# Performance work log

Hardware: AMD Instinct MI355X
Metric: run time of the kernel (lower is better)

## Reference

```python
import jax, jax.numpy as jnp
import numpy as np

D = 128      # input_dim (= out_channels = edge_dim)
H = 2        # n_head
N_ENT = 100000
B = 64       # number of queries / batches
R = 500      # number of relations
E = 400000   # number of original edges
NEG = 0.2    # GATv2 leaky_relu negative slope


def setup_inputs() -> dict:
    key = jax.random.key(0)
    ks = jax.random.split(key, 10)
    s = 1.0 / np.sqrt(D)
    queries = jax.random.normal(ks[0], (B, D), jnp.float32)
    entities = jax.random.normal(ks[1], (N_ENT, D), jnp.float32)
    edge_index = jax.random.randint(ks[2], (2, E), 0, N_ENT)
    relations = jax.random.normal(ks[3], (R, D), jnp.float32)
    relation_index = jax.random.randint(ks[4], (E,), 0, R)
    # guarantees batch.max()+1 == queries.shape[0] (module assert)
    batch = jnp.arange(N_ENT, dtype=jnp.int32) % B
    # GATv2Conv params: lin_l / lin_r (bias=True), lin_edge (bias=False), att, bias
    W_l = jax.random.normal(ks[5], (H * D, D), jnp.float32) * s
    b_l = jnp.zeros((H * D,), jnp.float32)
    W_r = jax.random.normal(ks[6], (H * D, D), jnp.float32) * s
    b_r = jnp.zeros((H * D,), jnp.float32)
    W_ea = jax.random.normal(ks[7], (H * D, D), jnp.float32) * s
    att = jax.random.normal(ks[8], (H, D), jnp.float32) * s
    bias = jnp.zeros((D,), jnp.float32)  # concat=False -> size out_channels
    # outer Injector.lin_edge: Linear(H*D, D, bias=True)
    W_le = jax.random.normal(ks[9], (D, H * D), jnp.float32) / np.sqrt(H * D)
    b_le = jnp.zeros((D,), jnp.float32)
    return dict(queries=queries, entities=entities, edge_index=edge_index,
                relations=relations, relation_index=relation_index, batch=batch,
                W_l=W_l, b_l=b_l, W_r=W_r, b_r=b_r, W_ea=W_ea, att=att,
                bias=bias, W_le=W_le, b_le=b_le)


def reference(queries, entities, edge_index, relations, relation_index, batch,
              W_l, b_l, W_r, b_r, W_ea, att, bias, W_le, b_le):
    n_ent = entities.shape[0]
    node = jnp.vstack([entities, queries])                        # [N+B, D]
    rel_feat = jnp.vstack([relations,
                           jnp.ones((1, relations.shape[1]), relations.dtype)])
    # added edges: query -> its entities
    src = jnp.concatenate([edge_index[0], batch.astype(edge_index.dtype) + n_ent])
    tgt = jnp.concatenate([edge_index[1],
                           jnp.arange(n_ent, dtype=edge_index.dtype)])
    rel_idx = jnp.concatenate([relation_index,
                               jnp.full((n_ent,), rel_feat.shape[0] - 1,
                                        relation_index.dtype)])
    edge_attr = rel_feat[rel_idx]                                  # [Etot, D]

    n_tot = node.shape[0]
    x_l = (node @ W_l.T + b_l).reshape(n_tot, H, D)                # source proj
    x_r = (node @ W_r.T + b_r).reshape(n_tot, H, D)                # target proj
    e = (edge_attr @ W_ea.T).reshape(-1, H, D)                     # [Etot, H, D]

    xj = x_l[src]                                                  # gather per edge
    z = jax.nn.leaky_relu(xj + x_r[tgt] + e, NEG)                  # [Etot, H, D]
    alpha = jnp.einsum('ehd,hd->eh', z, att)                       # [Etot, H]
    # segment softmax over target nodes
    amax = jax.ops.segment_max(alpha, tgt, num_segments=n_tot)
    alpha = jnp.exp(alpha - amax[tgt])
    denom = jax.ops.segment_sum(alpha, tgt, num_segments=n_tot)
    alpha = alpha / (denom[tgt] + 1e-16)

    msg = xj * alpha[..., None]                                    # [Etot, H, D]
    agg = jax.ops.segment_sum(msg, tgt, num_segments=n_tot)        # [Ntot, H, D]
    out = agg.mean(axis=1) + bias                                  # concat=False
    out_node = out[:n_ent]

    out_edge = jax.nn.relu(relations @ W_ea.T)                     # [R, H*D]
    out_edge = out_edge @ W_le.T + b_le                            # [R, D]
    return (out_node, out_edge)
```

## Files before the change

### kernel.cpp

```cpp
#include <hip/hip_runtime.h>
#include <math.h>

#define D 128
#define HD 256
#define N_ENT 100000
#define NBATCH 64
#define NTOT (N_ENT + NBATCH)
#define RCOUNT 500
#define E_BASE 400000
#define ETOT (E_BASE + N_ENT)
#define NEG 0.2f
#define SCAN_NB 391

typedef __attribute__((ext_vector_type(8))) short bf16x8;
typedef __attribute__((ext_vector_type(8))) unsigned short u16x8;
typedef __attribute__((ext_vector_type(4))) float f32x4;

static __device__ __forceinline__ unsigned short f2bf(float f) {
  unsigned u = __builtin_bit_cast(unsigned, f);
  u += 0x7fffu + ((u >> 16) & 1u);
  return (unsigned short)(u >> 16);
}
static __device__ __forceinline__ float bf2f(unsigned short h) {
  return __builtin_bit_cast(float, (unsigned)h << 16);
}

__global__ __launch_bounds__(256) void k_wcast(
    const float* __restrict__ W_l, const float* __restrict__ W_r,
    unsigned short* __restrict__ Wbf) {
  int idx = blockIdx.x * 256 + threadIdx.x;
  int e4 = idx * 4;
  int v = e4 >> 7;
  int k = e4 & 127;
  const float* src = (v < HD) ? (W_l + (size_t)v * D + k) : (W_r + (size_t)(v - HD) * D + k);
  float4 a = *(const float4*)src;
  *(ushort4*)(Wbf + (size_t)v * D + k) = make_ushort4(f2bf(a.x), f2bf(a.y), f2bf(a.z), f2bf(a.w));
}

__global__ __launch_bounds__(256) void k_rel(
    const float* __restrict__ relations, const float* __restrict__ W_ea,
    const float* __restrict__ W_le, const float* __restrict__ b_le,
    unsigned short* __restrict__ e_rel, float* __restrict__ out_edge) {
  __shared__ float relu_p[HD];
  int r = blockIdx.x;
  int j = threadIdx.x;
  const float* w = W_ea + (size_t)j * D;
  float acc = 0.f;
  if (r < RCOUNT) {
    const float* rel = relations + (size_t)r * D;
    for (int k = 0; k < D; k += 4) {
      float4 a = *(const float4*)(rel + k);
      float4 b = *(const float4*)(w + k);
      acc += a.x * b.x + a.y * b.y + a.z * b.z + a.w * b.w;
    }
  } else {
    for (int k = 0; k < D; k += 4) {
      float4 b = *(const float4*)(w + k);
      acc += b.x + b.y + b.z + b.w;
    }
  }
  e_rel[(size_t)r * HD + j] = f2bf(acc);
  if (r < RCOUNT) {
    relu_p[j] = acc > 0.f ? acc : 0.f;
    __syncthreads();
    if (j < D) {
      const float* wl = W_le + (size_t)j * HD;
      float o = b_le[j];
      for (int k = 0; k < HD; k += 4) {
        float4 p4 = *(const float4*)(relu_p + k);
        float4 w4 = *(const float4*)(wl + k);
        o += p4.x * w4.x + p4.y * w4.y + p4.z * w4.z + p4.w * w4.w;
      }
      out_edge[(size_t)r * D + j] = o;
    }
  }
}

#define LDA 136

__global__ __launch_bounds__(256) void k_gemm_mfma(
    const float* __restrict__ entities, const float* __restrict__ queries,
    const unsigned short* __restrict__ Wbf,
    const float* __restrict__ b_l, const float* __restrict__ b_r,
    unsigned short* __restrict__ x_l, unsigned short* __restrict__ x_r) {
  __shared__ unsigned short As[64 * LDA];
  __shared__ unsigned short Cs[64 * LDA];
  int rb = blockIdx.x;
  int gy = blockIdx.y;
  int tid = threadIdx.x;

  {
    int rr = tid >> 2;
    int part = (tid & 3) * 32;
    int row = rb * 64 + rr;
    const float* sp;
    if (row < N_ENT) sp = entities + (size_t)row * D;
    else if (row < NTOT) sp = queries + (size_t)(row - N_ENT) * D;
    else sp = entities;
#pragma unroll
    for (int k = 0; k < 32; k += 8) {
      float4 a0 = *(const float4*)(sp + part + k);
      float4 a1 = *(const float4*)(sp + part + k + 4);
      u16x8 p;
      p[0] = f2bf(a0.x); p[1] = f2bf(a0.y); p[2] = f2bf(a0.z); p[3] = f2bf(a0.w);
      p[4] = f2bf(a1.x); p[5] = f2bf(a1.y); p[6] = f2bf(a1.z); p[7] = f2bf(a1.w);
      *(u16x8*)(&As[rr * LDA + part + k]) = p;
    }
  }
  __syncthreads();

  int w = tid >> 6, lane = tid & 63;
  int wr = w >> 1, wc = w & 1;
  int m = lane & 15, q8 = (lane >> 4) * 8;
  const float* bv = gy ? b_r : b_l;
  unsigned short* xdst = gy ? x_r : x_l;

  for (int cc = 0; cc < 2; cc++) {
    f32x4 acc[2][4];
#pragma unroll
    for (int i = 0; i < 2; i++)
#pragma unroll
      for (int j = 0; j < 4; j++) acc[i][j] = (f32x4){0.f, 0.f, 0.f, 0.f};

    const unsigned short* wbase = Wbf + (size_t)(gy * 256 + cc * 128 + wc * 64 + m) * D;
#pragma unroll
    for (int ks = 0; ks < 128; ks += 32) {
      bf16x8 af[2], bfr[4];
#pragma unroll
      for (int i = 0; i < 2; i++)
        af[i] = *(const bf16x8*)(&As[(wr * 32 + i * 16 + m) * LDA + ks + q8]);
#pragma unroll
      for (int j = 0; j < 4; j++)
        bfr[j] = *(const bf16x8*)(wbase + (size_t)j * 16 * D + ks + q8);
#pragma unroll
      for (int i = 0; i < 2; i++)
#pragma unroll
        for (int j = 0; j < 4; j++)
          acc[i][j] = __builtin_amdgcn_mfma_f32_16x16x32_bf16(af[i], bfr[j], acc[i][j], 0, 0, 0);
    }

    __syncthreads();
#pragma unroll
    for (int j = 0; j < 4; j++) {
      int col = wc * 64 + j * 16 + m;
      float bb = bv[cc * 128 + col];
#pragma unroll
      for (int i = 0; i < 2; i++) {
        int row0 = wr * 32 + i * 16 + (lane >> 4) * 4;
#pragma unroll
        for (int r = 0; r < 4; r++)
          Cs[(row0 + r) * LDA + col] = f2bf(acc[i][j][r] + bb);
      }
    }
    __syncthreads();
#pragma unroll
    for (int it = 0; it < 4; it++) {
      int g = it * 256 + tid;
      int row = g >> 4, c8 = (g & 15) * 8;
      int grow = rb * 64 + row;
      if (grow < NTOT) {
        u16x8 v = *(const u16x8*)(&Cs[row * LDA + c8]);
        *(u16x8*)(xdst + (size_t)grow * HD + cc * 128 + c8) = v;
      }
    }
  }
}

__global__ void k_zero(int* __restrict__ counts) {
  int i = blockIdx.x * 256 + threadIdx.x;
  if (i < N_ENT) counts[i] = 0;
}

__global__ void k_hist(const int* __restrict__ edge_index, int* __restrict__ counts) {
  int e = blockIdx.x * 256 + threadIdx.x;
  if (e >= ETOT) return;
  int t = (e < E_BASE) ? edge_index[E_BASE + e] : (e - E_BASE);
  atomicAdd(counts + t, 1);
}

__global__ void k_scan1(const int* __restrict__ counts, int* __restrict__ bsum) {
  __shared__ int sdata[256];
  int i = blockIdx.x * 256 + threadIdx.x;
  sdata[threadIdx.x] = (i < N_ENT) ? counts[i] : 0;
  __syncthreads();
  for (int off = 128; off > 0; off >>= 1) {
    if (threadIdx.x < off) sdata[threadIdx.x] += sdata[threadIdx.x + off];
    __syncthreads();
  }
  if (threadIdx.x == 0) bsum[blockIdx.x] = sdata[0];
}

__global__ void k_scan2(const int* __restrict__ bsum, int* __restrict__ bpre) {
  __shared__ int s[512];
  int tid = threadIdx.x;
  s[tid] = (tid < SCAN_NB) ? bsum[tid] : 0;
  __syncthreads();
  for (int off = 1; off < 512; off <<= 1) {
    int y = (tid >= off) ? s[tid - off] : 0;
    __syncthreads();
    s[tid] += y;
    __syncthreads();
  }
  bpre[tid] = (tid == 0) ? 0 : s[tid - 1];
}

__global__ void k_scan3(const int* __restrict__ counts, const int* __restrict__ bpre,
                        int* __restrict__ offsets, int* __restrict__ cursor) {
  __shared__ int s[256];
  int tid = threadIdx.x;
  int i = blockIdx.x * 256 + tid;
  int v = (i < N_ENT) ? counts[i] : 0;
  s[tid] = v;
  __syncthreads();
  for (int off = 1; off < 256; off <<= 1) {
    int y = (tid >= off) ? s[tid - off] : 0;
    __syncthreads();
    s[tid] += y;
    __syncthreads();
  }
  int excl = bpre[blockIdx.x] + s[tid] - v;
  if (i <= N_ENT) offsets[i] = excl;
  if (i < N_ENT) cursor[i] = excl;
}

__global__ void k_scatter(const int* __restrict__ edge_index, const int* __restrict__ relation_index,
                          const int* __restrict__ batch, int* __restrict__ cursor,
                          unsigned int* __restrict__ sorted) {
  int e = blockIdx.x * 256 + threadIdx.x;
  if (e >= ETOT) return;
  int s, t, r;
  if (e < E_BASE) {
    s = edge_index[e];
    t = edge_index[E_BASE + e];
    r = relation_index[e];
  } else {
    int i = e - E_BASE;
    s = N_ENT + batch[i];
    t = i;
    r = RCOUNT;
  }
  int pos = atomicAdd(cursor + t, 1);
  sorted[pos] = (unsigned)s | ((unsigned)r << 17);
}

__global__ __launch_bounds__(256) void k_edge(
    const unsigned short* __restrict__ x_l, const unsigned short* __restrict__ x_r,
    const unsigned short* __restrict__ e_rel, const int* __restrict__ offsets,
    const unsigned int* __restrict__ sorted, const float* __restrict__ att,
    const float* __restrict__ bias, float* __restrict__ out) {
  int wv = threadIdx.x >> 6;
  int lane = threadIdx.x & 63;
  int t = blockIdx.x * 4 + wv;
  int elem = lane * 4;
  int d = elem & (D - 1);
  ushort4 xr4 = *(const ushort4*)(x_r + (size_t)t * HD + elem);
  float xrx = bf2f(xr4.x), xry = bf2f(xr4.y), xrz = bf2f(xr4.z), xrw = bf2f(xr4.w);
  float4 at = *(const float4*)(att + elem);
  int e0 = offsets[t], e1 = offsets[t + 1];
  float denom = 0.f;
  float4 acc = make_float4(0.f, 0.f, 0.f, 0.f);
  for (int e = e0; e < e1; e++) {
    unsigned sr = sorted[e];
    int s = sr & 0x1FFFF;
    int r = sr >> 17;
    ushort4 xl4 = *(const ushort4*)(x_l + (size_t)s * HD + elem);
    ushort4 er4 = *(const ushort4*)(e_rel + (size_t)r * HD + elem);
    float xlx = bf2f(xl4.x), xly = bf2f(xl4.y), xlz = bf2f(xl4.z), xlw = bf2f(xl4.w);
    float zx = xlx + xrx + bf2f(er4.x); zx = zx > 0.f ? zx : NEG * zx;
    float zy = xly + xry + bf2f(er4.y); zy = zy > 0.f ? zy : NEG * zy;
    float zz = xlz + xrz + bf2f(er4.z); zz = zz > 0.f ? zz : NEG * zz;
    float zw = xlw + xrw + bf2f(er4.w); zw = zw > 0.f ? zw : NEG * zw;
    float p = zx * at.x + zy * at.y + zz * at.z + zw * at.w;
    p += __shfl_xor(p, 1, 64);
    p += __shfl_xor(p, 2, 64);
    p += __shfl_xor(p, 4, 64);
    p += __shfl_xor(p, 8, 64);
    p += __shfl_xor(p, 16, 64);
    float wgt = __expf(p);
    denom += wgt;
    acc.x += wgt * xlx;
    acc.y += wgt * xly;
    acc.z += wgt * xlz;
    acc.w += wgt * xlw;
  }
  float inv = 1.f / (denom + 1e-16f);
  acc.x *= inv; acc.y *= inv; acc.z *= inv; acc.w *= inv;
  float ox = acc.x + __shfl_xor(acc.x, 32, 64);
  float oy = acc.y + __shfl_xor(acc.y, 32, 64);
  float oz = acc.z + __shfl_xor(acc.z, 32, 64);
  float ow = acc.w + __shfl_xor(acc.w, 32, 64);
  if (lane < 32) {
    float4 b4 = *(const float4*)(bias + d);
    *(float4*)(out + (size_t)t * D + d) =
        make_float4(ox * 0.5f + b4.x, oy * 0.5f + b4.y, oz * 0.5f + b4.z, ow * 0.5f + b4.w);
  }
}

extern "C" void kernel_launch(void* const* d_in, const int* in_sizes, int n_in,
                              void* d_out, int out_size, void* d_ws, size_t ws_size,
                              hipStream_t stream) {
  const float* queries = (const float*)d_in[0];
  const float* entities = (const float*)d_in[1];
  const int* edge_index = (const int*)d_in[2];
  const float* relations = (const float*)d_in[3];
  const int* relation_index = (const int*)d_in[4];
  const int* batch = (const int*)d_in[5];
  const float* W_l = (const float*)d_in[6];
  const float* b_l = (const float*)d_in[7];
  const float* W_r = (const float*)d_in[8];
  const float* b_r = (const float*)d_in[9];
  const float* W_ea = (const float*)d_in[10];
  const float* att = (const float*)d_in[11];
  const float* bias = (const float*)d_in[12];
  const float* W_le = (const float*)d_in[13];
  const float* b_le = (const float*)d_in[14];

  float* out_node = (float*)d_out;
  float* out_edge = out_node + (size_t)N_ENT * D;

  char* base = (char*)d_ws;
  size_t off = 0;
  auto take = [&](size_t nbytes) -> void* {
    void* p = base + off;
    off += (nbytes + 255) & ~(size_t)255;
    return p;
  };
  unsigned short* x_l = (unsigned short*)take((size_t)NTOT * HD * sizeof(unsigned short));
  unsigned short* x_r = (unsigned short*)take((size_t)NTOT * HD * sizeof(unsigned short));
  unsigned short* e_rel = (unsigned short*)take((size_t)(RCOUNT + 1) * HD * sizeof(unsigned short));
  unsigned short* Wbf = (unsigned short*)take((size_t)512 * D * sizeof(unsigned short));
  int* counts = (int*)take((size_t)N_ENT * sizeof(int));
  int* offsets = (int*)take((size_t)(N_ENT + 1) * sizeof(int));
  int* cursor = (int*)take((size_t)N_ENT * sizeof(int));
  int* bsum = (int*)take(512 * sizeof(int));
  int* bpre = (int*)take(512 * sizeof(int));
  unsigned int* sorted = (unsigned int*)take((size_t)ETOT * sizeof(unsigned int));

  k_wcast<<<dim3(64), dim3(256), 0, stream>>>(W_l, W_r, Wbf);
  k_rel<<<dim3(RCOUNT + 1), dim3(256), 0, stream>>>(relations, W_ea, W_le, b_le, e_rel, out_edge);
  k_gemm_mfma<<<dim3((NTOT + 63) / 64, 2), dim3(256), 0, stream>>>(entities, queries, Wbf, b_l, b_r, x_l, x_r);
  k_zero<<<dim3((N_ENT + 255) / 256), dim3(256), 0, stream>>>(counts);
  k_hist<<<dim3((ETOT + 255) / 256), dim3(256), 0, stream>>>(edge_index, counts);
  k_scan1<<<dim3(SCAN_NB), dim3(256), 0, stream>>>(counts, bsum);
  k_scan2<<<dim3(1), dim3(512), 0, stream>>>(bsum, bpre);
  k_scan3<<<dim3(SCAN_NB), dim3(256), 0, stream>>>(counts, bpre, offsets, cursor);
  k_scatter<<<dim3((ETOT + 255) / 256), dim3(256), 0, stream>>>(edge_index, relation_index, batch, cursor, sorted);
  k_edge<<<dim3(N_ENT / 4), dim3(256), 0, stream>>>(x_l, x_r, e_rel, offsets, sorted, att, bias, out_node);
}
```

Baseline: 334.4 us.

## Process two edges per wave in edge kernel and merge GEMM grid halves

The edge-attention kernel now splits each 64-lane wave into two halves. Each half handles a different edge with 8 elements per lane, so two edges are processed per iteration with wider 16-byte gathers and a shorter shuffle reduction. Partial sums from the two halves are combined at the end. The projection GEMM now computes both x_l and x_r in one block, so the converted input tile is loaded once instead of twice, at the cost of half as many blocks.

```diff
diff --git a/kernel.cpp b/kernel.cpp
--- a/kernel.cpp
+++ b/kernel.cpp
@@ -86,7 +86,6 @@
   __shared__ unsigned short As[64 * LDA];
   __shared__ unsigned short Cs[64 * LDA];
   int rb = blockIdx.x;
-  int gy = blockIdx.y;
   int tid = threadIdx.x;
 
   {
@@ -112,17 +111,20 @@
   int w = tid >> 6, lane = tid & 63;
   int wr = w >> 1, wc = w & 1;
   int m = lane & 15, q8 = (lane >> 4) * 8;
-  const float* bv = gy ? b_r : b_l;
-  unsigned short* xdst = gy ? x_r : x_l;
-
-  for (int cc = 0; cc < 2; cc++) {
+
+  for (int ccv = 0; ccv < 4; ccv++) {
+    bool isL = ccv < 2;
+    const float* bv = isL ? b_l : b_r;
+    unsigned short* xdst = isL ? x_l : x_r;
+    int cbase = (ccv & 1) * 128;
+
     f32x4 acc[2][4];
 #pragma unroll
     for (int i = 0; i < 2; i++)
 #pragma unroll
       for (int j = 0; j < 4; j++) acc[i][j] = (f32x4){0.f, 0.f, 0.f, 0.f};
 
-    const unsigned short* wbase = Wbf + (size_t)(gy * 256 + cc * 128 + wc * 64 + m) * D;
+    const unsigned short* wbase = Wbf + (size_t)(ccv * 128 + wc * 64 + m) * D;
 #pragma unroll
     for (int ks = 0; ks < 128; ks += 32) {
       bf16x8 af[2], bfr[4];
@@ -143,7 +145,7 @@
 #pragma unroll
     for (int j = 0; j < 4; j++) {
       int col = wc * 64 + j * 16 + m;
-      float bb = bv[cc * 128 + col];
+      float bb = bv[cbase + col];
 #pragma unroll
       for (int i = 0; i < 2; i++) {
         int row0 = wr * 32 + i * 16 + (lane >> 4) * 4;
@@ -160,7 +162,7 @@
       int grow = rb * 64 + row;
       if (grow < NTOT) {
         u16x8 v = *(const u16x8*)(&Cs[row * LDA + c8]);
-        *(u16x8*)(xdst + (size_t)grow * HD + cc * 128 + c8) = v;
+        *(u16x8*)(xdst + (size_t)grow * HD + cbase + c8) = v;
       }
     }
   }
@@ -251,48 +253,67 @@
   int wv = threadIdx.x >> 6;
   int lane = threadIdx.x & 63;
   int t = blockIdx.x * 4 + wv;
-  int elem = lane * 4;
-  int d = elem & (D - 1);
-  ushort4 xr4 = *(const ushort4*)(x_r + (size_t)t * HD + elem);
-  float xrx = bf2f(xr4.x), xry = bf2f(xr4.y), xrz = bf2f(xr4.z), xrw = bf2f(xr4.w);
-  float4 at = *(const float4*)(att + elem);
+  int half = lane >> 5;
+  int sl = lane & 31;
+  int elem = sl * 8;
+  u16x8 xr8 = *(const u16x8*)(x_r + (size_t)t * HD + elem);
+  float xr[8], at[8];
+#pragma unroll
+  for (int i = 0; i < 8; i++) xr[i] = bf2f(xr8[i]);
+  float4 at0 = *(const float4*)(att + elem);
+  float4 at1 = *(const float4*)(att + elem + 4);
+  at[0] = at0.x; at[1] = at0.y; at[2] = at0.z; at[3] = at0.w;
+  at[4] = at1.x; at[5] = at1.y; at[6] = at1.z; at[7] = at1.w;
   int e0 = offsets[t], e1 = offsets[t + 1];
   float denom = 0.f;
-  float4 acc = make_float4(0.f, 0.f, 0.f, 0.f);
-  for (int e = e0; e < e1; e++) {
-    unsigned sr = sorted[e];
+  float acc[8];
+#pragma unroll
+  for (int i = 0; i < 8; i++) acc[i] = 0.f;
+
+  for (int e = e0; e < e1; e += 2) {
+    int ee = e + half;
+    bool valid = ee < e1;
+    if (!valid) ee = e;
+    unsigned sr = sorted[ee];
     int s = sr & 0x1FFFF;
     int r = sr >> 17;
-    ushort4 xl4 = *(const ushort4*)(x_l + (size_t)s * HD + elem);
-    ushort4 er4 = *(const ushort4*)(e_rel + (size_t)r * HD + elem);
-    float xlx = bf2f(xl4.x), xly = bf2f(xl4.y), xlz = bf2f(xl4.z), xlw = bf2f(xl4.w);
-    float zx = xlx + xrx + bf2f(er4.x); zx = zx > 0.f ? zx : NEG * zx;
-    float zy = xly + xry + bf2f(er4.y); zy = zy > 0.f ? zy : NEG * zy;
-    float zz = xlz + xrz + bf2f(er4.z); zz = zz > 0.f ? zz : NEG * zz;
-    float zw = xlw + xrw + bf2f(er4.w); zw = zw > 0.f ? zw : NEG * zw;
-    float p = zx * at.x + zy * at.y + zz * at.z + zw * at.w;
+    u16x8 xl8 = *(const u16x8*)(x_l + (size_t)s * HD + elem);
+    u16x8 er8 = *(const u16x8*)(e_rel + (size_t)r * HD + elem);
+    float xl[8];
+    float p = 0.f;
+#pragma unroll
+    for (int i = 0; i < 8; i++) {
+      xl[i] = bf2f(xl8[i]);
+      float z = xl[i] + xr[i] + bf2f(er8[i]);
+      z = z > 0.f ? z : NEG * z;
+      p += z * at[i];
+    }
     p += __shfl_xor(p, 1, 64);
     p += __shfl_xor(p, 2, 64);
     p += __shfl_xor(p, 4, 64);
     p += __shfl_xor(p, 8, 64);
-    p += __shfl_xor(p, 16, 64);
-    float wgt = __expf(p);
+    float wgt = valid ? __expf(p) : 0.f;
     denom += wgt;
-    acc.x += wgt * xlx;
-    acc.y += wgt * xly;
-    acc.z += wgt * xlz;
-    acc.w += wgt * xlw;
-  }
+#pragma unroll
+    for (int i = 0; i < 8; i++) acc[i] += wgt * xl[i];
+  }
+  denom += __shfl_xor(denom, 32, 64);
+#pragma unroll
+  for (int i = 0; i < 8; i++) acc[i] += __shfl_xor(acc[i], 32, 64);
   float inv = 1.f / (denom + 1e-16f);
-  acc.x *= inv; acc.y *= inv; acc.z *= inv; acc.w *= inv;
-  float ox = acc.x + __shfl_xor(acc.x, 32, 64);
-  float oy = acc.y + __shfl_xor(acc.y, 32, 64);
-  float oz = acc.z + __shfl_xor(acc.z, 32, 64);
-  float ow = acc.w + __shfl_xor(acc.w, 32, 64);
-  if (lane < 32) {
-    float4 b4 = *(const float4*)(bias + d);
+  float o[8];
+#pragma unroll
+  for (int i = 0; i < 8; i++) o[i] = acc[i] * inv;
+#pragma unroll
+  for (int i = 0; i < 8; i++) o[i] += __shfl_xor(o[i], 16, 64);
+  if (lane < 16) {
+    int d = sl * 8;
+    float4 b0 = *(const float4*)(bias + d);
+    float4 b1 = *(const float4*)(bias + d + 4);
     *(float4*)(out + (size_t)t * D + d) =
-        make_float4(ox * 0.5f + b4.x, oy * 0.5f + b4.y, oz * 0.5f + b4.z, ow * 0.5f + b4.w);
+        make_float4(o[0] * 0.5f + b0.x, o[1] * 0.5f + b0.y, o[2] * 0.5f + b0.z, o[3] * 0.5f + b0.w);
+    *(float4*)(out + (size_t)t * D + d + 4) =
+        make_float4(o[4] * 0.5f + b1.x, o[5] * 0.5f + b1.y, o[6] * 0.5f + b1.z, o[7] * 0.5f + b1.w);
   }
 }
 
@@ -338,7 +359,7 @@
 
   k_wcast<<<dim3(64), dim3(256), 0, stream>>>(W_l, W_r, Wbf);
   k_rel<<<dim3(RCOUNT + 1), dim3(256), 0, stream>>>(relations, W_ea, W_le, b_le, e_rel, out_edge);
-  k_gemm_mfma<<<dim3((NTOT + 63) / 64, 2), dim3(256), 0, stream>>>(entities, queries, Wbf, b_l, b_r, x_l, x_r);
+  k_gemm_mfma<<<dim3((NTOT + 63) / 64), dim3(256), 0, stream>>>(entities, queries, Wbf, b_l, b_r, x_l, x_r);
   k_zero<<<dim3((N_ENT + 255) / 256), dim3(256), 0, stream>>>(counts);
   k_hist<<<dim3((ETOT + 255) / 256), dim3(256), 0, stream>>>(edge_index, counts);
   k_scan1<<<dim3(SCAN_NB), dim3(256), 0, stream>>>(counts, bsum);
```

Measured after the change: 319.2 us. 4.6% less time.
